# Performance work log

Hardware: AMD Instinct MI355X
Metric: run time of the kernel (lower is better)

## Reference

```python
import jax, jax.numpy as jnp
import numpy as np

NODE_N = 23
SEQ_LEN = 35
N_HEADS = 3
BN_EPS = 1e-5


def _normalize_digraph(A):
    # column-normalize: A @ diag(1/deg) (st-gcn tools.normalize_digraph)
    Dl = A.sum(0)
    inv = np.where(Dl > 0, 1.0 / np.where(Dl > 0, Dl, 1.0), 0.0)
    return A * inv[None, :]


def _build_A_ske():
    n = NODE_N
    bone = [[0, 2], [1, 2], [0, 3], [3, 6], [6, 9], [1, 4], [4, 7], [7, 10],
            [2, 5], [5, 8], [8, 12], [12, 15], [15, 17], [17, 19], [19, 21],
            [8, 13], [13, 16], [16, 18], [18, 20], [20, 22], [8, 11], [11, 14]]
    A_in = np.zeros((n, n), np.float64)
    A_out = np.zeros((n, n), np.float64)
    for i, j in bone:
        A_in[i, j] = 1.0
        A_out[j, i] = 1.0
    A_self = np.eye(n, dtype=np.float64)
    return np.stack([_normalize_digraph(A_in), _normalize_digraph(A_out), A_self]).astype(np.float32)


def setup_inputs() -> dict:
    key = jax.random.key(0)
    ks = jax.random.split(key, 12)
    b, c, o, n, l = 256, 64, 64, NODE_N, SEQ_LEN
    stdv = 1.0 / np.sqrt(n)           # reset_parameters: 1/sqrt(att.size(2)) = 1/sqrt(n)
    cbound = 1.0 / np.sqrt(c)         # conv2d 1x1 default init bound (fan_in = in_c)
    u = lambda k, shape, bnd: jax.random.uniform(k, shape, jnp.float32, -bnd, bnd)
    return {
        "x": jax.random.normal(ks[0], (b, c, n, l), jnp.float32),
        "cw1": u(ks[1], (N_HEADS, o, c), cbound),
        "cb1": u(ks[2], (N_HEADS, o), cbound),
        "cw2": u(ks[3], (N_HEADS, o, c), cbound),
        "cb2": u(ks[4], (N_HEADS, o), cbound),
        "bn_gamma": jnp.ones((N_HEADS, n * n), jnp.float32),
        "bn_beta": jnp.zeros((N_HEADS, n * n), jnp.float32),
        "mw": u(ks[5], (N_HEADS, o, c), cbound),
        "mb": u(ks[6], (N_HEADS, o), cbound),
        "att": jnp.full((N_HEADS, n, n), 1e-6, jnp.float32),
        "A_ske": jnp.asarray(_build_A_ske()),
        "weight_seq": u(ks[7], (l, l), stdv),
        "bias": u(ks[8], (l,), stdv),
    }


def reference(x, cw1, cb1, cw2, cb2, bn_gamma, bn_beta, mw, mb, att, A_ske, weight_seq, bias):
    b, c, n, l = x.shape
    o = cw1.shape[1]
    xp = jnp.transpose(x, (0, 1, 3, 2))                      # [b,c,l,n]

    # --- A_adp heads (vectorized across 3 heads) ---
    o1 = jnp.einsum('hoc,bcln->bholn', cw1, xp) + cb1[None, :, :, None, None]
    o2 = jnp.einsum('hoc,bcln->bholn', cw2, xp) + cb2[None, :, :, None, None]
    o1 = o1.reshape(b, N_HEADS, o * l, n)
    o2 = o2.reshape(b, N_HEADS, o * l, n)
    att_m = jnp.einsum('bhkm,bhkn->bhmn', o2, o1) / (o * l)  # [b,3,n,n]

    # BatchNorm1d over flattened n*n features, batch statistics (training mode)
    flat = att_m.reshape(b, N_HEADS, n * n)
    mean = flat.mean(axis=0)                                  # [3,n*n]
    var = flat.var(axis=0)                                    # biased, as torch BN
    flat = (flat - mean) / jnp.sqrt(var + BN_EPS) * bn_gamma + bn_beta
    A_adp = jax.nn.softmax(flat.reshape(b, N_HEADS, n, n), axis=-2)
    # dropout is identity in eval mode

    # --- graph convolution per head ---
    A = A_ske[None] + att[None] + A_adp                       # [b,3,n,n]
    support = jnp.einsum('bcln,bhnm->bhclm', xp, A)           # [b,3,c,l,n]
    head = jnp.einsum('hoc,bhclm->bholm', mw, support) + mb[None, :, :, None, None]
    gcn = jnp.transpose(head.sum(axis=1), (0, 1, 3, 2))       # [b,o,n,l]

    out = jnp.einsum('bonl,lm->bonm', gcn, weight_seq) + bias
    return out
```

## Files before the change

kernel.cpp:

```cpp
#include <hip/hip_runtime.h>
#include <hip/hip_bf16.h>

typedef __hip_bfloat16 bf16;
typedef __attribute__((ext_vector_type(8))) short bf16x8;
typedef __attribute__((ext_vector_type(4))) float f32x4;
typedef __attribute__((ext_vector_type(4))) unsigned short us4;
typedef __attribute__((ext_vector_type(8))) unsigned short us8;

#define NB   256
#define NN   23
#define NL   35
#define NNL  805
#define CNL  51520
#define NSQ  529
#define HF   1587
#define NCN  1472

#define OFF_W     0
#define OFF_U1    12288
#define OFF_U2    12480
#define OFF_S     12672
#define OFF_ATTM  12800
#define OFF_MEAN  419072
#define OFF_RSTD  420672
#define OFF_A     422272
#define OFF_MWH   828544
#define OFF_MWL   834688
#define OFF_MBS   840832
#define OFF_XTB   840960

__device__ inline unsigned short bfh(float x) {
    unsigned u = __float_as_uint(x);
    return (unsigned short)((u + 0x7FFFu + ((u >> 16) & 1u)) >> 16);
}
__device__ inline float bfh2f(unsigned short h) {
    return __uint_as_float(((unsigned)h) << 16);
}
__device__ inline unsigned short bf16rn(float x) {
    __hip_bfloat16 h = __float2bfloat16(x);
    return __builtin_bit_cast(unsigned short, h);
}

__global__ __launch_bounds__(1024) void k_xt(const float* __restrict__ x,
                                             float* __restrict__ ws) {
    int b = blockIdx.x, t = threadIdx.x;
    __shared__ float sx[64 * 23 * 18];
    const float* xb = x + b * CNL;
    unsigned short* xo = (unsigned short*)(ws + OFF_XTB) + (size_t)b * NL * 2944;
    for (int lh = 0; lh < 2; lh++) {
        int l0 = lh * 18, Lc = lh ? 17 : 18;
        if (lh) __syncthreads();
        for (int i = t; i < 1472 * Lc; i += 1024) {
            int cn = i / Lc, li = i - cn * Lc;
            sx[cn * 18 + li] = xb[cn * 35 + l0 + li];
        }
        __syncthreads();
        for (int item = t; item < 184 * Lc; item += 1024) {
            int li = item / 184, rem = item - li * 184;
            int n = rem >> 3, k = rem & 7;
            us8 hi, lo;
            #pragma unroll
            for (int e = 0; e < 8; e++) {
                float v = sx[((8 * k + e) * 23 + n) * 18 + li];
                unsigned short hb = bfh(v);
                hi[e] = hb;
                lo[e] = bfh(v - bfh2f(hb));
            }
            unsigned short* dst = xo + (size_t)(l0 + li) * 2944 + n * 64 + 8 * k;
            *(us8*)(dst) = hi;
            *(us8*)(dst + 1472) = lo;
        }
    }
}

__global__ __launch_bounds__(256) void k_prep(const float* __restrict__ cw1,
                                              const float* __restrict__ cb1,
                                              const float* __restrict__ cw2,
                                              const float* __restrict__ cb2,
                                              const float* __restrict__ mw,
                                              const float* __restrict__ mb,
                                              float* __restrict__ ws) {
    int h = blockIdx.x, t = threadIdx.x;
    __shared__ float s1[4096], s2[4096];
    if (h < 3) {
        for (int i = t; i < 4096; i += 256) {
            s1[i] = cw1[h * 4096 + i];
            s2[i] = cw2[h * 4096 + i];
        }
        __syncthreads();
        for (int i = t; i < 4096; i += 256) {
            int c2 = i >> 6, c1 = i & 63;
            float acc = 0.f;
            for (int o = 0; o < 64; o++) acc += s2[o * 64 + c2] * s1[o * 64 + c1];
            ws[OFF_W + h * 4096 + i] = acc;
        }
        if (t < 64) {
            float a = 0.f, b2 = 0.f;
            for (int o = 0; o < 64; o++) {
                a  += cb2[h * 64 + o] * s1[o * 64 + t];
                b2 += cb1[h * 64 + o] * s2[o * 64 + t];
            }
            ws[OFF_U1 + h * 64 + t] = a;
            ws[OFF_U2 + h * 64 + t] = b2;
        }
        if (t == 0) {
            float a = 0.f;
            for (int o = 0; o < 64; o++) a += cb1[h * 64 + o] * cb2[h * 64 + o];
            ws[OFF_S + h] = a;
        }
    } else {
        unsigned short* mh = (unsigned short*)(ws + OFF_MWH);
        unsigned short* ml = (unsigned short*)(ws + OFF_MWL);
        for (int i = t; i < 12288; i += 256) {
            float v = mw[i];
            unsigned short hb = bfh(v);
            mh[i] = hb;
            ml[i] = bfh(v - bfh2f(hb));
        }
        if (t < 64) ws[OFF_MBS + t] = mb[t] + mb[64 + t] + mb[128 + t];
    }
}

__global__ __launch_bounds__(256) void k_attm(float* __restrict__ ws) {
    const int b = blockIdx.x, h = blockIdx.y, t = threadIdx.x;
    const int lane = t & 63;
    const int w = __builtin_amdgcn_readfirstlane(t >> 6);
    const int lg = lane >> 4;
    const int lr = lane & 15;

    __shared__ unsigned short sXh[2][32 * 72];
    __shared__ unsigned short sXl[2][32 * 72];
    __shared__ unsigned short sPh[32 * 72];
    __shared__ unsigned short sPl[32 * 72];
    __shared__ float sxs[64 * 25];
    __shared__ float sA1[23], sA2[23];

    const unsigned short* xthl = (const unsigned short*)(ws + OFF_XTB);

    bf16x8 wh[2], wl[2];
    {
        const float* Wg = ws + OFF_W + h * 4096 + (16 * w + lr) * 64;
        #pragma unroll
        for (int s = 0; s < 2; s++) {
            const float* p = Wg + 32 * s + 8 * lg;
            float4 v0 = *(const float4*)(p);
            float4 v1 = *(const float4*)(p + 4);
            float vv[8] = {v0.x, v0.y, v0.z, v0.w, v1.x, v1.y, v1.z, v1.w};
            #pragma unroll
            for (int e = 0; e < 8; e++) {
                unsigned short hb = bfh(vv[e]);
                wh[s][e] = (short)hb;
                wl[s][e] = (short)bfh(vv[e] - bfh2f(hb));
            }
        }
    }

    const int j1 = t;
    const int p1 = j1 / 184, r1 = j1 - p1 * 184;
    const int n1 = r1 >> 3, k1 = r1 & 7;
    unsigned short* d1 = (p1 ? sXl[0] : sXh[0]) + n1 * 72 + 8 * k1;
    const int j2 = 256 + t;
    const int r2 = j2 - 184;
    const int n2 = r2 >> 3, k2 = r2 & 7;
    unsigned short* d2 = sXl[0] + n2 * 72 + 8 * k2;

    const int mt = w >> 1, nt = w & 1;
    f32x4 attC = {0.f, 0.f, 0.f, 0.f};
    float xa1[8] = {0, 0, 0, 0, 0, 0, 0, 0};
    float xa2[8] = {0, 0, 0, 0, 0, 0, 0, 0};

    {
        const us8* g = (const us8*)(xthl + (size_t)(b * NL) * 2944);
        us8 v1 = g[j1];
        *(us8*)(d1) = v1;
        #pragma unroll
        for (int e = 0; e < 8; e++) xa1[e] += bfh2f(v1[e]);
        if (t < 112) {
            us8 v2 = g[j2];
            *(us8*)(d2) = v2;
            #pragma unroll
            for (int e = 0; e < 8; e++) xa2[e] += bfh2f(v2[e]);
        }
    }

    #pragma unroll 1
    for (int l = 0; l < NL; l++) {
        const int cur = l & 1;
        __syncthreads();

        us8 vn1, vn2;
        if (l < NL - 1) {
            const us8* g = (const us8*)(xthl + (size_t)(b * NL + l + 1) * 2944);
            vn1 = g[j1];
            if (t < 112) vn2 = g[j2];
        }

        const unsigned short* xh = sXh[cur];
        const unsigned short* xl = sXl[cur];

        f32x4 pc[2];
        #pragma unroll
        for (int ntt = 0; ntt < 2; ntt++) {
            f32x4 c = {0.f, 0.f, 0.f, 0.f};
            #pragma unroll
            for (int s = 0; s < 2; s++) {
                int off = (ntt * 16 + lr) * 72 + 32 * s + 8 * lg;
                bf16x8 bh = *(const bf16x8*)(xh + off);
                bf16x8 bl = *(const bf16x8*)(xl + off);
                c = __builtin_amdgcn_mfma_f32_16x16x32_bf16(wh[s], bh, c, 0, 0, 0);
                c = __builtin_amdgcn_mfma_f32_16x16x32_bf16(wh[s], bl, c, 0, 0, 0);
                c = __builtin_amdgcn_mfma_f32_16x16x32_bf16(wl[s], bh, c, 0, 0, 0);
            }
            pc[ntt] = c;
        }
        #pragma unroll
        for (int ntt = 0; ntt < 2; ntt++) {
            int n = ntt * 16 + lr;
            int c2 = 16 * w + 4 * lg;
            us4 ph4, pl4;
            #pragma unroll
            for (int r = 0; r < 4; r++) {
                float v = pc[ntt][r];
                unsigned short hb = bf16rn(v);
                ph4[r] = hb;
                pl4[r] = bf16rn(v - bfh2f(hb));
            }
            *(us4*)(sPh + n * 72 + c2) = ph4;
            *(us4*)(sPl + n * 72 + c2) = pl4;
        }

        if (l < NL - 1) {
            *(us8*)(d1 + (cur ^ 1) * 2304) = vn1;
            #pragma unroll
            for (int e = 0; e < 8; e++) xa1[e] += bfh2f(vn1[e]);
            if (t < 112) {
                *(us8*)(d2 + (cur ^ 1) * 2304) = vn2;
                #pragma unroll
                for (int e = 0; e < 8; e++) xa2[e] += bfh2f(vn2[e]);
            }
        }
        __syncthreads();

        #pragma unroll
        for (int s = 0; s < 2; s++) {
            int aoff = (mt * 16 + lr) * 72 + 32 * s + 8 * lg;
            int boff = (nt * 16 + lr) * 72 + 32 * s + 8 * lg;
            bf16x8 ah = *(const bf16x8*)(xh + aoff);
            bf16x8 al = *(const bf16x8*)(xl + aoff);
            bf16x8 bh = *(const bf16x8*)(sPh + boff);
            bf16x8 bl = *(const bf16x8*)(sPl + boff);
            attC = __builtin_amdgcn_mfma_f32_16x16x32_bf16(ah, bh, attC, 0, 0, 0);
            attC = __builtin_amdgcn_mfma_f32_16x16x32_bf16(ah, bl, attC, 0, 0, 0);
            attC = __builtin_amdgcn_mfma_f32_16x16x32_bf16(al, bh, attC, 0, 0, 0);
        }
    }

    if (t < 184) {
        #pragma unroll
        for (int e = 0; e < 8; e++) sxs[(8 * k1 + e) * 25 + n1] = xa1[e];
    }
    __syncthreads();
    if (t >= 184) {
        #pragma unroll
        for (int e = 0; e < 8; e++) sxs[(8 * k1 + e) * 25 + n1] += xa1[e];
    }
    if (t < 112) {
        #pragma unroll
        for (int e = 0; e < 8; e++) sxs[(8 * k2 + e) * 25 + n2] += xa2[e];
    }
    __syncthreads();
    if (t < 23) {
        float a = 0.f;
        const float* u = ws + OFF_U1 + h * 64;
        for (int c = 0; c < 64; c++) a += u[c] * sxs[c * 25 + t];
        sA1[t] = a;
    } else if (t >= 32 && t < 55) {
        int n = t - 32;
        float a = 0.f;
        const float* u = ws + OFF_U2 + h * 64;
        for (int c = 0; c < 64; c++) a += u[c] * sxs[c * 25 + n];
        sA2[n] = a;
    }
    __syncthreads();

    float sh = ws[OFF_S + h];
    float* o = ws + OFF_ATTM + (size_t)b * HF + h * NSQ;
    int n = nt * 16 + lr;
    if (n < 23) {
        #pragma unroll
        for (int r = 0; r < 4; r++) {
            int m = mt * 16 + 4 * lg + r;
            if (m < 23)
                o[m * 23 + n] = (attC[r] + sA1[n] + sA2[m] + 35.f * sh) * (1.f / 2240.f);
        }
    }
}

__global__ __launch_bounds__(512) void k_bn(float* __restrict__ ws) {
    int t = threadIdx.x;
    int fi = t & 63, bg = t >> 6;
    int f = blockIdx.x * 64 + fi;
    __shared__ float rs[8][64], rs2[8][64];
    float s = 0.f, s2 = 0.f;
    if (f < HF) {
        const float* p = ws + OFF_ATTM + f + (size_t)bg * 32 * HF;
        for (int b = 0; b < 32; b++) {
            float v = p[b * HF];
            s += v; s2 += v * v;
        }
    }
    rs[bg][fi] = s; rs2[bg][fi] = s2;
    __syncthreads();
    if (bg == 0 && f < HF) {
        float ts = 0.f, ts2 = 0.f;
        #pragma unroll
        for (int g = 0; g < 8; g++) { ts += rs[g][fi]; ts2 += rs2[g][fi]; }
        float mean = ts * (1.f / 256.f);
        float var  = ts2 * (1.f / 256.f) - mean * mean;
        ws[OFF_MEAN + f] = mean;
        ws[OFF_RSTD + f] = rsqrtf(var + 1e-5f);
    }
}

__global__ __launch_bounds__(256) void k_adp(const float* __restrict__ gamma,
                                             const float* __restrict__ beta,
                                             const float* __restrict__ att,
                                             const float* __restrict__ aske,
                                             float* __restrict__ ws) {
    int b = blockIdx.x, h = blockIdx.y, t = threadIdx.x;
    __shared__ float sv[529];
    const float* am   = ws + OFF_ATTM + b * HF + h * NSQ;
    const float* mean = ws + OFF_MEAN + h * NSQ;
    const float* rstd = ws + OFF_RSTD + h * NSQ;
    for (int i = t; i < 529; i += 256) {
        sv[i] = (am[i] - mean[i]) * rstd[i] * gamma[h * NSQ + i] + beta[h * NSQ + i];
    }
    __syncthreads();
    if (t < 23) {
        float mx = -1e30f;
        #pragma unroll
        for (int m = 0; m < 23; m++) mx = fmaxf(mx, sv[m * 23 + t]);
        float e[23];
        float sum = 0.f;
        #pragma unroll
        for (int m = 0; m < 23; m++) {
            float v = __expf(sv[m * 23 + t] - mx);
            e[m] = v; sum += v;
        }
        float inv = 1.f / sum;
        #pragma unroll
        for (int m = 0; m < 23; m++) sv[m * 23 + t] = e[m] * inv;
    }
    __syncthreads();
    float* o = ws + OFF_A + b * HF + h * NSQ;
    for (int i = t; i < 529; i += 256) {
        o[i] = sv[i] + aske[h * NSQ + i] + att[h * NSQ + i];
    }
}

#define SYS 38
#define STS 44
__global__ __launch_bounds__(512, 2) void k_fused(float* __restrict__ ws,
                                                  const float* __restrict__ wseq,
                                                  const float* __restrict__ biasp,
                                                  float* __restrict__ out) {
    const int b = blockIdx.x, t = threadIdx.x;
    const int lane = t & 63;
    const int w = __builtin_amdgcn_readfirstlane(t >> 6);
    const int lg = lane >> 4, lr = lane & 15;
    const int nt = w >> 2, ot = w & 3;
    const int ot2 = w >> 1, mt = w & 1;

    __shared__ __align__(16) unsigned short sXh[32 * 72], sXl[32 * 72];
    __shared__ __align__(16) unsigned short sAT[3][2][32 * 40];
    __shared__ __align__(16) unsigned short sT[3][64 * STS];
    __shared__ __align__(16) unsigned short sY[1472 * SYS];
    __shared__ __align__(16) unsigned short sWTh[48 * 40], sWTl[48 * 40];
    __shared__ float sWt[3 * 35];
    __shared__ float sBias[35];

    const unsigned short* xthl = (const unsigned short*)(ws + OFF_XTB);
    const float* Ab  = ws + OFF_A + (size_t)b * HF;

    for (int i = t; i < 9 * 72; i += 512) {
        sXh[23 * 72 + i] = 0;
        sXl[23 * 72 + i] = 0;
    }
    for (int i = t; i < 3 * 1280; i += 512) {
        int h = i / 1280, r2 = i - h * 1280, m = r2 / 40, n = r2 - m * 40;
        float v = (n < 23 && m < 23) ? Ab[h * 529 + n * 23 + m] : 0.f;
        unsigned short hb = bfh(v);
        sAT[h][0][m * 40 + n] = hb;
        sAT[h][1][m * 40 + n] = bfh(v - bfh2f(hb));
    }
    for (int i = t; i < 48 * 40; i += 512) {
        int lp = i / 40, l = i - lp * 40;
        float v = (lp < 35 && l < 32) ? wseq[l * 35 + lp] : 0.f;
        unsigned short hb = bfh(v);
        sWTh[i] = hb;
        sWTl[i] = bfh(v - bfh2f(hb));
    }
    if (t < 105) sWt[t] = wseq[(32 + t / 35) * 35 + (t % 35)];
    if (t >= 128 && t < 163) sBias[t - 128] = biasp[t - 128];

    const unsigned short* mwh = (const unsigned short*)(ws + OFF_MWH);
    const unsigned short* mwl = (const unsigned short*)(ws + OFF_MWL);
    bf16x8 fwh[3][2], fwl[3][2];
    #pragma unroll
    for (int h = 0; h < 3; h++)
        #pragma unroll
        for (int s = 0; s < 2; s++) {
            int off = h * 4096 + (16 * ot + lr) * 64 + 32 * s + 8 * lg;
            fwh[h][s] = *(const bf16x8*)(mwh + off);
            fwl[h][s] = *(const bf16x8*)(mwl + off);
        }
    float4 mbsv = *(const float4*)(ws + OFF_MBS + 16 * ot2 + 4 * lg);
    float mb4[4] = {mbsv.x, mbsv.y, mbsv.z, mbsv.w};

    const int p1 = t / 184, r1 = t - p1 * 184;
    const int n1 = r1 >> 3, k1 = r1 & 7;
    unsigned short* d1 = (p1 ? sXl : sXh) + n1 * 72 + 8 * k1;

    const f32x4 zf = {0.f, 0.f, 0.f, 0.f};

    if (t < 368) {
        const us8* g = (const us8*)(xthl + (size_t)(b * NL) * 2944);
        *(us8*)d1 = g[t];
    }

    #pragma unroll 1
    for (int l = 0; l < NL; l++) {
        __syncthreads();

        us8 vn;
        if (l < NL - 1 && t < 368) {
            const us8* g = (const us8*)(xthl + (size_t)(b * NL + l + 1) * 2944);
            vn = g[t];
        }

        bf16x8 xh0 = *(const bf16x8*)(sXh + (16 * nt + lr) * 72 + 8 * lg);
        bf16x8 xh1 = *(const bf16x8*)(sXh + (16 * nt + lr) * 72 + 32 + 8 * lg);
        bf16x8 xl0 = *(const bf16x8*)(sXl + (16 * nt + lr) * 72 + 8 * lg);
        bf16x8 xl1 = *(const bf16x8*)(sXl + (16 * nt + lr) * 72 + 32 + 8 * lg);
        #pragma unroll
        for (int h = 0; h < 3; h++) {
            f32x4 cH = __builtin_amdgcn_mfma_f32_16x16x32_bf16(xh0, fwh[h][0], zf, 0, 0, 0);
            cH = __builtin_amdgcn_mfma_f32_16x16x32_bf16(xh1, fwh[h][1], cH, 0, 0, 0);
            f32x4 cC = __builtin_amdgcn_mfma_f32_16x16x32_bf16(xh0, fwl[h][0], zf, 0, 0, 0);
            cC = __builtin_amdgcn_mfma_f32_16x16x32_bf16(xh1, fwl[h][1], cC, 0, 0, 0);
            cC = __builtin_amdgcn_mfma_f32_16x16x32_bf16(xl0, fwh[h][0], cC, 0, 0, 0);
            cC = __builtin_amdgcn_mfma_f32_16x16x32_bf16(xl1, fwh[h][1], cC, 0, 0, 0);
            us4 t4;
            #pragma unroll
            for (int r = 0; r < 4; r++) t4[r] = bf16rn(cH[r] + cC[r]);
            *(us4*)(&sT[h][(16 * ot + lr) * STS + 16 * nt + 4 * lg]) = t4;
        }
        __syncthreads();

        f32x4 Yh = zf, Yc = zf;
        #pragma unroll
        for (int h = 0; h < 3; h++) {
            union { bf16x8 v; us4 q[2]; } tu;
            tu.q[0] = *(const us4*)(&sT[h][(16 * ot2 + lr) * STS + 8 * lg]);
            tu.q[1] = *(const us4*)(&sT[h][(16 * ot2 + lr) * STS + 8 * lg + 4]);
            bf16x8 ah = *(const bf16x8*)(&sAT[h][0][(16 * mt + lr) * 40 + 8 * lg]);
            bf16x8 al = *(const bf16x8*)(&sAT[h][1][(16 * mt + lr) * 40 + 8 * lg]);
            Yh = __builtin_amdgcn_mfma_f32_16x16x32_bf16(tu.v, ah, Yh, 0, 0, 0);
            Yc = __builtin_amdgcn_mfma_f32_16x16x32_bf16(tu.v, al, Yc, 0, 0, 0);
        }
        int m = 16 * mt + lr;
        if (m < 23) {
            #pragma unroll
            for (int r = 0; r < 4; r++) {
                int o = 16 * ot2 + 4 * lg + r;
                float yv = Yh[r] + Yc[r] + mb4[r];
                sY[(o * 23 + m) * SYS + l] = bf16rn(yv);
            }
        }

        if (l < NL - 1 && t < 368) *(us8*)d1 = vn;
    }
    __syncthreads();

    #pragma unroll 1
    for (int tt = w; tt < 276; tt += 8) {
        int pt = tt / 3, lt = tt - pt * 3;
        int pA = 16 * pt + lr;
        const unsigned short* yb = sY + pA * SYS + 8 * lg;
        union { bf16x8 v; unsigned u[4]; } au;
        au.u[0] = *(const unsigned*)(yb);
        au.u[1] = *(const unsigned*)(yb + 2);
        au.u[2] = *(const unsigned*)(yb + 4);
        au.u[3] = *(const unsigned*)(yb + 6);
        bf16x8 wbh = *(const bf16x8*)(sWTh + (16 * lt + lr) * 40 + 8 * lg);
        bf16x8 wbl = *(const bf16x8*)(sWTl + (16 * lt + lr) * 40 + 8 * lg);
        f32x4 c0 = __builtin_amdgcn_mfma_f32_16x16x32_bf16(au.v, wbh, zf, 0, 0, 0);
        f32x4 c1 = __builtin_amdgcn_mfma_f32_16x16x32_bf16(au.v, wbl, zf, 0, 0, 0);
        int lpc = 16 * lt + lr;
        if (lpc < 35) {
            float wt0 = sWt[lpc], wt1 = sWt[35 + lpc], wt2 = sWt[70 + lpc];
            float bv = sBias[lpc];
            #pragma unroll
            for (int r = 0; r < 4; r++) {
                int pr = 16 * pt + 4 * lg + r;
                const unsigned short* yt = sY + pr * SYS + 32;
                unsigned t0 = *(const unsigned*)(yt);
                unsigned t1 = *(const unsigned*)(yt + 2);
                float v = c0[r] + c1[r] + bv
                        + bfh2f((unsigned short)(t0 & 0xffff)) * wt0
                        + bfh2f((unsigned short)(t0 >> 16))    * wt1
                        + bfh2f((unsigned short)(t1 & 0xffff)) * wt2;
                out[((size_t)b * 1472 + pr) * 35 + lpc] = v;
            }
        }
    }
}

extern "C" void kernel_launch(void* const* d_in, const int* in_sizes, int n_in,
                              void* d_out, int out_size, void* d_ws, size_t ws_size,
                              hipStream_t stream) {
    const float* x    = (const float*)d_in[0];
    const float* cw1  = (const float*)d_in[1];
    const float* cb1  = (const float*)d_in[2];
    const float* cw2  = (const float*)d_in[3];
    const float* cb2  = (const float*)d_in[4];
    const float* gam  = (const float*)d_in[5];
    const float* bet  = (const float*)d_in[6];
    const float* mw   = (const float*)d_in[7];
    const float* mb   = (const float*)d_in[8];
    const float* att  = (const float*)d_in[9];
    const float* aske = (const float*)d_in[10];
    const float* wsq  = (const float*)d_in[11];
    const float* bias = (const float*)d_in[12];
    float* ws = (float*)d_ws;
    float* out = (float*)d_out;

    hipLaunchKernelGGL(k_prep, dim3(4),       dim3(256),  0, stream, cw1, cb1, cw2, cb2, mw, mb, ws);
    hipLaunchKernelGGL(k_xt,   dim3(256),     dim3(1024), 0, stream, x, ws);
    hipLaunchKernelGGL(k_attm, dim3(256, 3),  dim3(256),  0, stream, ws);
    hipLaunchKernelGGL(k_bn,   dim3(25),      dim3(512),  0, stream, ws);
    hipLaunchKernelGGL(k_adp,  dim3(256, 3),  dim3(256),  0, stream, gam, bet, att, aske, ws);
    hipLaunchKernelGGL(k_fused, dim3(256),    dim3(512),  0, stream, ws, wsq, bias, out);
}
```

Baseline: 253.0 us.

## Accumulate sequence projection in registers instead of staging Y in LDS

```diff
diff --git a/kernel.cpp b/kernel.cpp
--- a/kernel.cpp
+++ b/kernel.cpp
@@ -358,7 +358,6 @@
     }
 }
 
-#define SYS 38
 #define STS 44
 __global__ __launch_bounds__(512, 2) void k_fused(float* __restrict__ ws,
                                                   const float* __restrict__ wseq,
@@ -374,10 +373,7 @@
     __shared__ __align__(16) unsigned short sXh[32 * 72], sXl[32 * 72];
     __shared__ __align__(16) unsigned short sAT[3][2][32 * 40];
     __shared__ __align__(16) unsigned short sT[3][64 * STS];
-    __shared__ __align__(16) unsigned short sY[1472 * SYS];
-    __shared__ __align__(16) unsigned short sWTh[48 * 40], sWTl[48 * 40];
-    __shared__ float sWt[3 * 35];
-    __shared__ float sBias[35];
+    __shared__ __align__(16) float sEp[16 * 23 * 36];
 
     const unsigned short* xthl = (const unsigned short*)(ws + OFF_XTB);
     const float* Ab  = ws + OFF_A + (size_t)b * HF;
@@ -393,15 +389,6 @@
         sAT[h][0][m * 40 + n] = hb;
         sAT[h][1][m * 40 + n] = bfh(v - bfh2f(hb));
     }
-    for (int i = t; i < 48 * 40; i += 512) {
-        int lp = i / 40, l = i - lp * 40;
-        float v = (lp < 35 && l < 32) ? wseq[l * 35 + lp] : 0.f;
-        unsigned short hb = bfh(v);
-        sWTh[i] = hb;
-        sWTl[i] = bfh(v - bfh2f(hb));
-    }
-    if (t < 105) sWt[t] = wseq[(32 + t / 35) * 35 + (t % 35)];
-    if (t >= 128 && t < 163) sBias[t - 128] = biasp[t - 128];
 
     const unsigned short* mwh = (const unsigned short*)(ws + OFF_MWH);
     const unsigned short* mwl = (const unsigned short*)(ws + OFF_MWL);
@@ -422,6 +409,12 @@
     unsigned short* d1 = (p1 ? sXl : sXh) + n1 * 72 + 8 * k1;
 
     const f32x4 zf = {0.f, 0.f, 0.f, 0.f};
+
+    float acc[4][35];
+    #pragma unroll
+    for (int r = 0; r < 4; r++)
+        #pragma unroll
+        for (int lp = 0; lp < 35; lp++) acc[r][lp] = 0.f;
 
     if (t < 368) {
         const us8* g = (const us8*)(xthl + (size_t)(b * NL) * 2944);
@@ -468,50 +461,40 @@
             Yh = __builtin_amdgcn_mfma_f32_16x16x32_bf16(tu.v, ah, Yh, 0, 0, 0);
             Yc = __builtin_amdgcn_mfma_f32_16x16x32_bf16(tu.v, al, Yc, 0, 0, 0);
         }
-        int m = 16 * mt + lr;
+
+        float yv0 = Yh[0] + Yc[0] + mb4[0];
+        float yv1 = Yh[1] + Yc[1] + mb4[1];
+        float yv2 = Yh[2] + Yc[2] + mb4[2];
+        float yv3 = Yh[3] + Yc[3] + mb4[3];
+        const float* wr = wseq + l * 35;
+        #pragma unroll
+        for (int lp = 0; lp < 35; lp++) {
+            float wv = wr[lp];
+            acc[0][lp] += yv0 * wv;
+            acc[1][lp] += yv1 * wv;
+            acc[2][lp] += yv2 * wv;
+            acc[3][lp] += yv3 * wv;
+        }
+
+        if (l < NL - 1 && t < 368) *(us8*)d1 = vn;
+    }
+
+    const int oi = 4 * ot2 + lg;
+    const int m  = 16 * mt + lr;
+    #pragma unroll 1
+    for (int r = 0; r < 4; r++) {
+        __syncthreads();
         if (m < 23) {
-            #pragma unroll
-            for (int r = 0; r < 4; r++) {
-                int o = 16 * ot2 + 4 * lg + r;
-                float yv = Yh[r] + Yc[r] + mb4[r];
-                sY[(o * 23 + m) * SYS + l] = bf16rn(yv);
-            }
-        }
-
-        if (l < NL - 1 && t < 368) *(us8*)d1 = vn;
-    }
-    __syncthreads();
-
-    #pragma unroll 1
-    for (int tt = w; tt < 276; tt += 8) {
-        int pt = tt / 3, lt = tt - pt * 3;
-        int pA = 16 * pt + lr;
-        const unsigned short* yb = sY + pA * SYS + 8 * lg;
-        union { bf16x8 v; unsigned u[4]; } au;
-        au.u[0] = *(const unsigned*)(yb);
-        au.u[1] = *(const unsigned*)(yb + 2);
-        au.u[2] = *(const unsigned*)(yb + 4);
-        au.u[3] = *(const unsigned*)(yb + 6);
-        bf16x8 wbh = *(const bf16x8*)(sWTh + (16 * lt + lr) * 40 + 8 * lg);
-        bf16x8 wbl = *(const bf16x8*)(sWTl + (16 * lt + lr) * 40 + 8 * lg);
-        f32x4 c0 = __builtin_amdgcn_mfma_f32_16x16x32_bf16(au.v, wbh, zf, 0, 0, 0);
-        f32x4 c1 = __builtin_amdgcn_mfma_f32_16x16x32_bf16(au.v, wbl, zf, 0, 0, 0);
-        int lpc = 16 * lt + lr;
-        if (lpc < 35) {
-            float wt0 = sWt[lpc], wt1 = sWt[35 + lpc], wt2 = sWt[70 + lpc];
-            float bv = sBias[lpc];
-            #pragma unroll
-            for (int r = 0; r < 4; r++) {
-                int pr = 16 * pt + 4 * lg + r;
-                const unsigned short* yt = sY + pr * SYS + 32;
-                unsigned t0 = *(const unsigned*)(yt);
-                unsigned t1 = *(const unsigned*)(yt + 2);
-                float v = c0[r] + c1[r] + bv
-                        + bfh2f((unsigned short)(t0 & 0xffff)) * wt0
-                        + bfh2f((unsigned short)(t0 >> 16))    * wt1
-                        + bfh2f((unsigned short)(t1 & 0xffff)) * wt2;
-                out[((size_t)b * 1472 + pr) * 35 + lpc] = v;
-            }
+            float* ep = sEp + (oi * 23 + m) * 36;
+            #pragma unroll
+            for (int lp = 0; lp < 35; lp++) ep[lp] = acc[r][lp] + biasp[lp];
+        }
+        __syncthreads();
+        for (int i = t; i < 16 * 805; i += 512) {
+            int o16 = i / 805, rem = i - o16 * 805;
+            int mm = rem / 35, lp = rem - mm * 35;
+            out[((size_t)(b * 1472 + (4 * o16 + r) * 23)) * 35 + rem] =
+                sEp[(o16 * 23 + mm) * 36 + lp];
         }
     }
 }
```

Result: slower. 603.8 us (+138.6%).
